# Kernel optimization log

Measured on AMD Instinct MI355X. Metric: run time of the kernel, lower is better.

Reference implementation:

```python
import jax, jax.numpy as jnp
import numpy as np

DIM = 2048
NUM_HEADS = 16
HEAD_DIM = DIM // NUM_HEADS  # 128
BATCH = 2
SEQ = 2048


def rope(x):
    # x: [B, S, H, Dh]; interleaved even/odd rotary embedding
    B, S, H, Dh = x.shape
    inv_freq = 1.0 / (10000.0 ** (jnp.arange(0, Dh, 2, dtype=jnp.float32) / Dh))  # [Dh/2]
    freqs = jnp.arange(S, dtype=jnp.float32)[:, None] * inv_freq[None, :]         # [S, Dh/2]
    cos = jnp.cos(freqs)[None, :, None, :]  # [1, S, 1, Dh/2]
    sin = jnp.sin(freqs)[None, :, None, :]
    x_even = x[..., 0::2]
    x_odd = x[..., 1::2]
    r_even = x_even * cos - x_odd * sin
    r_odd = x_even * sin + x_odd * cos
    # interleave back: [..., Dh/2, 2] -> [..., Dh]
    return jnp.stack([r_even, r_odd], axis=-1).reshape(x.shape)


def setup_inputs() -> dict:
    key = jax.random.key(0)
    ks = jax.random.split(key, 5)
    s = 1.0 / np.sqrt(DIM)
    return {
        "x": jax.random.normal(ks[0], (BATCH, SEQ, DIM), dtype=jnp.float32),
        "wq": jax.random.normal(ks[1], (DIM, DIM), dtype=jnp.float32) * s,
        "wk": jax.random.normal(ks[2], (DIM, DIM), dtype=jnp.float32) * s,
        "wv": jax.random.normal(ks[3], (DIM, DIM), dtype=jnp.float32) * s,
        "wo": jax.random.normal(ks[4], (DIM, DIM), dtype=jnp.float32) * s,
    }


def reference(x, wq, wk, wv, wo):
    B, S, D = x.shape
    H, Dh = NUM_HEADS, HEAD_DIM
    scale = Dh ** -0.5
    # nn.Linear(bias=False): y = x @ W.T
    q = (x @ wq.T).reshape(B, S, H, Dh)
    k = (x @ wk.T).reshape(B, S, H, Dh)
    v = (x @ wv.T).reshape(B, S, H, Dh)
    q = rope(q)
    k = rope(k)
    # no kv_cache -> new cache is (k, v) in [B, S, H, Dh] layout
    attn = jnp.einsum("bqhd,bkhd->bhqk", q, k) * scale  # [B, H, S, S]
    attn = jax.nn.softmax(attn, axis=-1)
    out = jnp.einsum("bhqk,bkhd->bqhd", attn, v).reshape(B, S, D)
    out = out @ wo.T
    return (out, k, v)
```

## Files before the change

kernel.cpp:

```cpp
#include <hip/hip_runtime.h>
#include <hip/hip_bf16.h>

#define DIM 2048
#define SEQLEN 2048
#define NHEADS 16
#define HDIM 128
#define NBATCH 2

using short8 = __attribute__((ext_vector_type(8))) short;
using f32x4 = __attribute__((ext_vector_type(4))) float;
using ushort4v = __attribute__((ext_vector_type(4))) unsigned short;

typedef __attribute__((address_space(1))) const void gvoid_t;
typedef __attribute__((address_space(3))) void lvoid_t;

__device__ __forceinline__ void gl_lds16(const void* g, void* l) {
  __builtin_amdgcn_global_load_lds((gvoid_t*)g, (lvoid_t*)l, 16, 0, 0);
}

__device__ __forceinline__ unsigned short f2bf(float f) {
  union { float f; unsigned int u; } v;
  v.f = f;
  unsigned int u = v.u;
  return (unsigned short)((u + 0x7FFFu + ((u >> 16) & 1u)) >> 16);
}

__device__ __forceinline__ f32x4 mfma16(short8 a, short8 b, f32x4 c) {
  return __builtin_amdgcn_mfma_f32_16x16x32_bf16(a, b, c, 0, 0, 0);
}

__global__ __launch_bounds__(256) void cast_all(
    const float4* __restrict__ x,
    const float4* __restrict__ wq, const float4* __restrict__ wk,
    const float4* __restrict__ wv, const float4* __restrict__ wo,
    ushort4v* __restrict__ xb,
    ushort4v* __restrict__ wqb, ushort4v* __restrict__ wkb,
    ushort4v* __restrict__ wvb, ushort4v* __restrict__ wob)
{
  const long NXV = 2097152;
  const long NWV = 1048576;
  long tid = (long)blockIdx.x * blockDim.x + threadIdx.x;
  long nth = (long)gridDim.x * blockDim.x;
  for (long i = tid; i < NXV + 4 * NWV; i += nth) {
    const float4* s; ushort4v* dst; long off;
    if (i < NXV) { s = x; dst = xb; off = i; }
    else {
      long j = i - NXV;
      int w = (int)(j >> 20);
      off = j & (NWV - 1);
      switch (w) {
        case 0:  s = wq; dst = wqb; break;
        case 1:  s = wk; dst = wkb; break;
        case 2:  s = wv; dst = wvb; break;
        default: s = wo; dst = wob; break;
      }
    }
    float4 f = s[off];
    ushort4v u;
    u.x = f2bf(f.x); u.y = f2bf(f.y); u.z = f2bf(f.z); u.w = f2bf(f.w);
    dst[off] = u;
  }
}

__global__ __launch_bounds__(256) void rope_tables(float* __restrict__ ctab,
                                                   float* __restrict__ stab)
{
  int idx = blockIdx.x * 256 + threadIdx.x;
  if (idx >= SEQLEN * 64) return;
  int s = idx >> 6, i = idx & 63;
  float inv = powf(10000.0f, -(float)(2 * i) * (1.0f / 128.0f));
  float a = (float)s * inv;
  ctab[idx] = cosf(a);
  stab[idx] = sinf(a);
}

template<bool ROPE, bool WF32, bool WBF16>
__global__ __launch_bounds__(256) void gemm_bt(
    const unsigned short* __restrict__ A,
    const unsigned short* __restrict__ B,
    float* __restrict__ Cf,
    unsigned short* __restrict__ Cb,
    int M, int N, int K,
    const float* __restrict__ ctab,
    const float* __restrict__ stab,
    float premul)
{
  __shared__ unsigned short As[2][128 * 64];
  __shared__ unsigned short Bs[2][128 * 64];
  const int tid = threadIdx.x;
  const int wv = tid >> 6;
  const int lane = tid & 63;
  const int q4 = lane >> 4;
  const int l15 = lane & 15;
  const int m0 = blockIdx.y * 128;
  const int n0 = blockIdx.x * 128;
  const int wy = wv >> 1, wx = wv & 1;

  f32x4 acc[4][4];
  for (int i = 0; i < 4; ++i)
    for (int j = 0; j < 4; ++j)
      acc[i][j] = f32x4{0.f, 0.f, 0.f, 0.f};

  auto stage = [&](int buf, int k0) {
    for (int j = 0; j < 4; ++j) {
      int sb = j * 256 + wv * 64;
      int slot = sb + lane;
      int row = slot >> 3, cp = slot & 7;
      int c = cp ^ (row & 7);
      gl_lds16(A + (size_t)(m0 + row) * K + k0 + c * 8, &As[buf][sb * 8]);
      gl_lds16(B + (size_t)(n0 + row) * K + k0 + c * 8, &Bs[buf][sb * 8]);
    }
  };

  stage(0, 0);
  __syncthreads();

  int cur = 0;
  for (int k0 = 0; k0 < K; k0 += 64) {
    if (k0 + 64 < K) stage(cur ^ 1, k0 + 64);

    short8 af[2][4], bf[2][4];
    for (int s = 0; s < 2; ++s)
      for (int i = 0; i < 4; ++i) {
        int row = wy * 64 + i * 16 + l15;
        int c = (s * 4 + q4) ^ (row & 7);
        af[s][i] = *reinterpret_cast<const short8*>(&As[cur][row * 64 + c * 8]);
      }
    for (int s = 0; s < 2; ++s)
      for (int j = 0; j < 4; ++j) {
        int row = wx * 64 + j * 16 + l15;
        int c = (s * 4 + q4) ^ (row & 7);
        bf[s][j] = *reinterpret_cast<const short8*>(&Bs[cur][row * 64 + c * 8]);
      }
    for (int s = 0; s < 2; ++s)
      for (int i = 0; i < 4; ++i)
        for (int j = 0; j < 4; ++j)
          acc[i][j] = mfma16(af[s][i], bf[s][j], acc[i][j]);

    __syncthreads();
    cur ^= 1;
  }

  for (int i = 0; i < 4; ++i) {
    for (int j = 0; j < 4; ++j) {
      int colb = n0 + wx * 64 + j * 16 + l15;
      for (int r = 0; r < 4; ++r) {
        int row = m0 + wy * 64 + i * 16 + q4 * 4 + r;
        float val = acc[i][j][r];
        if (ROPE) {
          int s = row & (SEQLEN - 1);
          int pi = (colb & (HDIM - 1)) >> 1;
          float cs = ctab[(s << 6) + pi];
          float sn = stab[(s << 6) + pi];
          float partner = __shfl_xor(val, 1);
          val = (colb & 1) ? fmaf(partner, sn, val * cs)
                           : fmaf(val, cs, -partner * sn);
        }
        if (WF32) Cf[(size_t)row * N + colb] = val;
        if (WBF16) Cb[(size_t)row * N + colb] = f2bf(val * premul);
      }
    }
  }
}

__global__ __launch_bounds__(256) void transpose_v(const float* __restrict__ v,
                                                   unsigned short* __restrict__ vt)
{
  __shared__ float tile[64][65];
  const int b = blockIdx.z;
  const int s0 = blockIdx.y * 64;
  const int d0 = blockIdx.x * 64;
  const int tx = threadIdx.x & 63;
  const int ty = threadIdx.x >> 6;
  for (int r = 0; r < 16; ++r) {
    int srow = r * 4 + ty;
    tile[srow][tx] = v[((size_t)(b * SEQLEN + s0 + srow)) * DIM + d0 + tx];
  }
  __syncthreads();
  for (int r = 0; r < 16; ++r) {
    int drow = r * 4 + ty;
    int d = d0 + drow;
    int bh = b * NHEADS + (d >> 7);
    int dh = d & 127;
    vt[((size_t)(bh * HDIM + dh)) * SEQLEN + s0 + tx] = f2bf(tile[tx][drow]);
  }
}

__global__ __launch_bounds__(256, 4) void flash_attn(
    const unsigned short* __restrict__ qb,
    const unsigned short* __restrict__ kb,
    const unsigned short* __restrict__ vt,
    unsigned short* __restrict__ ab)
{
  __shared__ unsigned short KP[64 * 128];
  __shared__ unsigned short VTs[128 * 64];
  __shared__ unsigned short Ps[64 * 64];
  const int tid = threadIdx.x;
  const int wvi = tid >> 6;
  const int lane = tid & 63;
  const int q4 = lane >> 4;
  const int l15 = lane & 15;
  const int bh = blockIdx.x;
  const int q0 = blockIdx.y * 64;
  const int b = bh >> 4, h = bh & 15;

  const unsigned short* qbase = qb + (size_t)b * SEQLEN * DIM + h * HDIM;
  const unsigned short* kbase = kb + (size_t)b * SEQLEN * DIM + h * HDIM;
  const unsigned short* vbase = vt + (size_t)bh * HDIM * SEQLEN;

  short8 qf[4];
  {
    const unsigned short* qrow = qbase + (size_t)(q0 + wvi * 16 + l15) * DIM;
    for (int ks = 0; ks < 4; ++ks)
      qf[ks] = *reinterpret_cast<const short8*>(qrow + (ks * 4 + q4) * 8);
  }

  float m_run[4], l_run[4];
  f32x4 o[8];
  for (int r = 0; r < 4; ++r) { m_run[r] = -3.0e38f; l_run[r] = 0.f; }
  for (int ct = 0; ct < 8; ++ct) o[ct] = f32x4{0.f, 0.f, 0.f, 0.f};

  const int par = lane & 1;

  for (int kv = 0; kv < SEQLEN / 64; ++kv) {
    const int kv0 = kv * 64;
    for (int j = 0; j < 4; ++j) {
      int sb = wvi * 256 + j * 64;
      int slot = sb + lane;
      {
        int row = slot >> 4, cp = slot & 15;
        int c = cp ^ (row & 7);
        gl_lds16(kbase + (size_t)(kv0 + row) * DIM + c * 8, &KP[sb * 8]);
      }
      {
        int row = slot >> 3, cp = slot & 7;
        int c = cp ^ (row & 7);
        gl_lds16(vbase + (size_t)row * SEQLEN + kv0 + c * 8, &VTs[sb * 8]);
      }
    }
    __syncthreads();

    f32x4 sc[4];
    for (int ct = 0; ct < 4; ++ct) sc[ct] = f32x4{0.f, 0.f, 0.f, 0.f};
    for (int ct = 0; ct < 4; ++ct) {
      int kr = ct * 16 + l15;
      for (int ks = 0; ks < 4; ++ks) {
        int c = (ks * 4 + q4) ^ (kr & 7);
        short8 kf = *reinterpret_cast<const short8*>(&KP[kr * 128 + c * 8]);
        sc[ct] = mfma16(qf[ks], kf, sc[ct]);
      }
    }

    float lm[4];
    for (int r = 0; r < 4; ++r)
      lm[r] = fmaxf(fmaxf(sc[0][r], sc[1][r]), fmaxf(sc[2][r], sc[3][r]));
    bool grow = false;
    for (int r = 0; r < 4; ++r) grow |= (lm[r] > m_run[r] + 8.0f);
    if (__any(grow)) {
      for (int r = 0; r < 4; ++r) {
        float mx = lm[r];
        for (int d = 1; d < 16; d <<= 1) mx = fmaxf(mx, __shfl_xor(mx, d));
        float mnew = fmaxf(m_run[r], mx);
        float al = __builtin_amdgcn_exp2f(m_run[r] - mnew);
        m_run[r] = mnew;
        l_run[r] *= al;
        for (int ct = 0; ct < 8; ++ct) o[ct][r] *= al;
      }
    }

    for (int ct = 0; ct < 4; ++ct)
      for (int r = 0; r < 4; ++r) {
        float e = __builtin_amdgcn_exp2f(sc[ct][r] - m_run[r]);
        sc[ct][r] = e;
        l_run[r] += e;
      }

    for (int ct = 0; ct < 4; ++ct) {
      float t0 = __shfl_xor(sc[ct][0], 1);
      float t1 = __shfl_xor(sc[ct][1], 1);
      float t2 = __shfl_xor(sc[ct][2], 1);
      float t3 = __shfl_xor(sc[ct][3], 1);
      float a0 = par ? t2 : sc[ct][0];
      float b0 = par ? sc[ct][2] : t0;
      float a1 = par ? t3 : sc[ct][1];
      float b1 = par ? sc[ct][3] : t1;
      unsigned int pk0, pk1;
      asm("v_cvt_pk_bf16_f32 %0, %1, %2" : "=v"(pk0) : "v"(a0), "v"(b0));
      asm("v_cvt_pk_bf16_f32 %0, %1, %2" : "=v"(pk1) : "v"(a1), "v"(b1));
      int col0 = ct * 16 + (l15 & ~1);
      int prow0 = wvi * 16 + q4 * 4 + par * 2;
      int c0 = (col0 >> 3) ^ (prow0 & 7);
      *reinterpret_cast<unsigned int*>(&Ps[prow0 * 64 + c0 * 8 + (col0 & 7)]) = pk0;
      int prow1 = prow0 + 1;
      int c1 = (col0 >> 3) ^ (prow1 & 7);
      *reinterpret_cast<unsigned int*>(&Ps[prow1 * 64 + c1 * 8 + (col0 & 7)]) = pk1;
    }
    __asm__ volatile("s_waitcnt lgkmcnt(0)" ::: "memory");

    short8 pf[2];
    {
      int prow = wvi * 16 + l15;
      for (int ks = 0; ks < 2; ++ks) {
        int c = (ks * 4 + q4) ^ (prow & 7);
        pf[ks] = *reinterpret_cast<const short8*>(&Ps[prow * 64 + c * 8]);
      }
    }
    for (int ct = 0; ct < 8; ++ct) {
      int vr = ct * 16 + l15;
      for (int ks = 0; ks < 2; ++ks) {
        int c = (ks * 4 + q4) ^ (vr & 7);
        short8 vf = *reinterpret_cast<const short8*>(&VTs[vr * 64 + c * 8]);
        o[ct] = mfma16(pf[ks], vf, o[ct]);
      }
    }
    __syncthreads();
  }

  for (int r = 0; r < 4; ++r) {
    float t = l_run[r];
    for (int d = 1; d < 16; d <<= 1) t += __shfl_xor(t, d);
    float invl = 1.0f / t;
    int qrow = q0 + wvi * 16 + q4 * 4 + r;
    size_t base = ((size_t)(b * SEQLEN) + qrow) * DIM + h * HDIM;
    for (int ct = 0; ct < 8; ++ct)
      ab[base + ct * 16 + l15] = f2bf(o[ct][r] * invl);
  }
}

extern "C" void kernel_launch(void* const* d_in, const int* in_sizes, int n_in,
                              void* d_out, int out_size, void* d_ws, size_t ws_size,
                              hipStream_t stream) {
  const float* x  = (const float*)d_in[0];
  const float* wq = (const float*)d_in[1];
  const float* wk = (const float*)d_in[2];
  const float* wv = (const float*)d_in[3];
  const float* wo = (const float*)d_in[4];

  float* outp = (float*)d_out;
  float* kout = outp + 8388608;
  float* vout = outp + 16777216;

  unsigned short* ws  = (unsigned short*)d_ws;
  unsigned short* xb  = ws;
  unsigned short* wqb = xb + 8388608;
  unsigned short* wkb = wqb + 4194304;
  unsigned short* wvb = wkb + 4194304;
  unsigned short* wob = wvb + 4194304;
  unsigned short* qb  = wob + 4194304;
  unsigned short* kb  = qb + 8388608;
  unsigned short* vtb = kb + 8388608;
  unsigned short* abuf = vtb + 8388608;
  float* ctab = (float*)(abuf + 8388608);
  float* stab = ctab + 131072;

  cast_all<<<2048, 256, 0, stream>>>(
      (const float4*)x, (const float4*)wq, (const float4*)wk,
      (const float4*)wv, (const float4*)wo,
      (ushort4v*)xb, (ushort4v*)wqb, (ushort4v*)wkb,
      (ushort4v*)wvb, (ushort4v*)wob);
  rope_tables<<<512, 256, 0, stream>>>(ctab, stab);

  dim3 gg(16, 32);
  const float qscale = 0.08838834764831845f * 1.4426950408889634f;
  gemm_bt<true,  false, true ><<<gg, 256, 0, stream>>>(xb, wqb, nullptr, qb, 4096, 2048, 2048, ctab, stab, qscale);
  gemm_bt<true,  true,  true ><<<gg, 256, 0, stream>>>(xb, wkb, kout,    kb, 4096, 2048, 2048, ctab, stab, 1.0f);
  gemm_bt<false, true,  false><<<gg, 256, 0, stream>>>(xb, wvb, vout, nullptr, 4096, 2048, 2048, ctab, stab, 1.0f);

  transpose_v<<<dim3(32, 32, 2), 256, 0, stream>>>(vout, vtb);
  flash_attn<<<dim3(32, 32), 256, 0, stream>>>(qb, kb, vtb, abuf);

  gemm_bt<false, true,  false><<<gg, 256, 0, stream>>>(abuf, wob, outp, nullptr, 4096, 2048, 2048, ctab, stab, 1.0f);
}
```

Baseline: 462.7 us.

## Prefetch next K/V tile into registers during attention compute

Replaces the per-iteration direct global-to-LDS loads of K and V, which were followed by a barrier, with a register prefetch of the next tile issued before the QK and PV MFMAs. After compute, a barrier is taken and the prefetched registers are written into LDS. The goal is to hide global memory latency behind the matrix math. It also raises wave priority around the MFMA loops with s_setprio. The cost is more VGPRs for the prefetch buffers, which may reduce occupancy, plus an extra barrier per iteration.

After: 505.5 us. +9.2%, slower.

```diff
diff --git a/kernel.cpp b/kernel.cpp
--- a/kernel.cpp
+++ b/kernel.cpp
@@ -222,26 +222,42 @@
 
   const int par = lane & 1;
 
+  for (int j = 0; j < 4; ++j) {
+    int sb = wvi * 256 + j * 64;
+    int slot = sb + lane;
+    {
+      int row = slot >> 4, cp = slot & 15;
+      int c = cp ^ (row & 7);
+      gl_lds16(kbase + (size_t)row * DIM + c * 8, &KP[sb * 8]);
+    }
+    {
+      int row = slot >> 3, cp = slot & 7;
+      int c = cp ^ (row & 7);
+      gl_lds16(vbase + (size_t)row * SEQLEN + c * 8, &VTs[sb * 8]);
+    }
+  }
+  __syncthreads();
+
   for (int kv = 0; kv < SEQLEN / 64; ++kv) {
-    const int kv0 = kv * 64;
-    for (int j = 0; j < 4; ++j) {
-      int sb = wvi * 256 + j * 64;
-      int slot = sb + lane;
-      {
-        int row = slot >> 4, cp = slot & 15;
-        int c = cp ^ (row & 7);
-        gl_lds16(kbase + (size_t)(kv0 + row) * DIM + c * 8, &KP[sb * 8]);
-      }
-      {
-        int row = slot >> 3, cp = slot & 7;
-        int c = cp ^ (row & 7);
-        gl_lds16(vbase + (size_t)row * SEQLEN + kv0 + c * 8, &VTs[sb * 8]);
-      }
-    }
-    __syncthreads();
+    short8 kreg[4], vreg[4];
+    const int nkv0 = kv * 64 + 64;
+    const bool pre = (kv + 1 < SEQLEN / 64);
+    if (pre) {
+#pragma unroll
+      for (int j = 0; j < 4; ++j) {
+        int slot = wvi * 256 + j * 64 + lane;
+        int krow = slot >> 4, kc = (slot & 15) ^ (krow & 7);
+        kreg[j] = *reinterpret_cast<const short8*>(
+            kbase + (size_t)(nkv0 + krow) * DIM + kc * 8);
+        int vrow = slot >> 3, vc = (slot & 7) ^ (vrow & 7);
+        vreg[j] = *reinterpret_cast<const short8*>(
+            vbase + (size_t)vrow * SEQLEN + nkv0 + vc * 8);
+      }
+    }
 
     f32x4 sc[4];
     for (int ct = 0; ct < 4; ++ct) sc[ct] = f32x4{0.f, 0.f, 0.f, 0.f};
+    __builtin_amdgcn_s_setprio(1);
     for (int ct = 0; ct < 4; ++ct) {
       int kr = ct * 16 + l15;
       for (int ks = 0; ks < 4; ++ks) {
@@ -250,6 +266,7 @@
         sc[ct] = mfma16(qf[ks], kf, sc[ct]);
       }
     }
+    __builtin_amdgcn_s_setprio(0);
 
     float lm[4];
     for (int r = 0; r < 4; ++r)
@@ -305,12 +322,24 @@
         pf[ks] = *reinterpret_cast<const short8*>(&Ps[prow * 64 + c * 8]);
       }
     }
+    __builtin_amdgcn_s_setprio(1);
     for (int ct = 0; ct < 8; ++ct) {
       int vr = ct * 16 + l15;
       for (int ks = 0; ks < 2; ++ks) {
         int c = (ks * 4 + q4) ^ (vr & 7);
         short8 vf = *reinterpret_cast<const short8*>(&VTs[vr * 64 + c * 8]);
         o[ct] = mfma16(pf[ks], vf, o[ct]);
+      }
+    }
+    __builtin_amdgcn_s_setprio(0);
+
+    __syncthreads();
+    if (pre) {
+#pragma unroll
+      for (int j = 0; j < 4; ++j) {
+        int slot = wvi * 256 + j * 64 + lane;
+        *reinterpret_cast<short8*>(&KP[slot * 8]) = kreg[j];
+        *reinterpret_cast<short8*>(&VTs[slot * 8]) = vreg[j];
       }
     }
     __syncthreads();
```
